# Performance work log

Hardware: AMD Instinct MI355X
Metric: run time of the kernel (lower is better)

Reference implementation:

```python
import jax, jax.numpy as jnp
import numpy as np

EPS = 1e-12  # torch F.normalize default eps


def l2_normalize_c(x):
    # F.normalize over channel dim (dim=1): x / max(||x||_2, eps)
    nrm = jnp.sqrt(jnp.sum(x * x, axis=1, keepdims=True))
    return x / jnp.maximum(nrm, EPS)


def resize_bilinear_ac(x, H, W):
    # bilinear, align_corners=True (matches torch F.interpolate)
    n, c, h, w = x.shape
    ys = jnp.linspace(0.0, h - 1.0, H)
    xs = jnp.linspace(0.0, w - 1.0, W)
    y0 = jnp.floor(ys).astype(jnp.int32)
    y1 = jnp.minimum(y0 + 1, h - 1)
    wy = (ys - y0.astype(ys.dtype))[:, None]          # [H,1]
    x0 = jnp.floor(xs).astype(jnp.int32)
    x1 = jnp.minimum(x0 + 1, w - 1)
    wx = xs - x0.astype(xs.dtype)                      # [W]
    rows = x[:, :, y0, :] * (1.0 - wy) + x[:, :, y1, :] * wy   # [n,c,H,w]
    return rows[:, :, :, x0] * (1.0 - wx) + rows[:, :, :, x1] * wx  # [n,c,H,W]


def unfold_3x3_d2(x):
    # nn.Unfold(kernel=3, dilation=2, padding=2, stride=1) viewed as [n,c,9,h,w]
    n, c, h, w = x.shape
    xp = jnp.pad(x, ((0, 0), (0, 0), (2, 2), (2, 2)))
    return jnp.stack(
        [xp[:, :, dy:dy + h, dx:dx + w] for dy in (0, 2, 4) for dx in (0, 2, 4)],
        axis=2,
    )  # [n,c,9,h,w], kernel index row-major (ky*3+kx) matching torch unfold


def setup_inputs() -> dict:
    key = jax.random.key(0)
    k1, k2, k3, k4, k5 = jax.random.split(key, 5)
    return {
        "c1": jax.random.normal(k1, (4, 256, 128, 128), dtype=jnp.float32),
        "c2": jax.random.normal(k2, (4, 512, 64, 64), dtype=jnp.float32),
        "out": jax.random.normal(k3, (4, 256, 64, 64), dtype=jnp.float32),
        "w_refine": jax.random.normal(k4, (32, 256), dtype=jnp.float32) * 0.05,
        "w_refine2": jax.random.normal(k5, (32, 512), dtype=jnp.float32) * 0.05,
    }


def reference(c1, c2, out, w_refine, w_refine2):
    n, _, h, w = c1.shape
    # 1x1 conv (no bias) + L2 normalize over channels
    q = l2_normalize_c(jnp.einsum("nchw,kc->nkhw", c1, w_refine))       # [n,32,h,w]
    c2u = resize_bilinear_ac(c2, h, w)
    kft = l2_normalize_c(jnp.einsum("nchw,kc->nkhw", c2u, w_refine2))    # [n,32,h,w]
    kpat = unfold_3x3_d2(kft)                                            # [n,32,9,h,w]
    energy = jnp.einsum("nchw,nckhw->nkhw", q, kpat)                     # [n,9,h,w]
    att = jax.nn.softmax(energy, axis=1)
    outu = resize_bilinear_ac(out, h, w)                                 # [n,C,h,w]
    vpat = unfold_3x3_d2(outu)                                           # [n,C,9,h,w]
    return jnp.einsum("nkhw,nckhw->nchw", att, vpat)
```

## Files before the change

### kernel.cpp

```cpp
#include <hip/hip_runtime.h>
#include <hip/hip_bf16.h>


typedef float f32x4 __attribute__((ext_vector_type(4)));
typedef float f32x2 __attribute__((ext_vector_type(2)));

#define SCL (63.0f / 127.0f)

__global__ __launch_bounds__(512) void k_q(const float* __restrict__ c1,
                                           const float* __restrict__ wr,
                                           float* __restrict__ q) {
    __shared__ float red[4 * 32 * 130];
    int b = blockIdx.x;
    int n = b >> 7;
    int pblk = (b & 127) * 128;
    int t = threadIdx.x;
    int lane = t & 63;
    int w = t >> 6;
    int cg = __builtin_amdgcn_readfirstlane(w & 3);
    int og = __builtin_amdgcn_readfirstlane(w >> 2);

    const float* src = c1 + ((size_t)n * 256 + cg * 64) * 16384 + pblk + lane * 2;
    const float* wp  = wr + (og * 16) * 256 + cg * 64;

    float acc0[16], acc1[16];
#pragma unroll
    for (int o = 0; o < 16; ++o) { acc0[o] = 0.f; acc1[o] = 0.f; }
#pragma unroll 4
    for (int c = 0; c < 64; ++c) {
        f32x2 v = *(const f32x2*)(src + (size_t)c * 16384);
#pragma unroll
        for (int o = 0; o < 16; ++o) {
            float wv = wp[o * 256 + c];
            acc0[o] = fmaf(v[0], wv, acc0[o]);
            acc1[o] = fmaf(v[1], wv, acc1[o]);
        }
    }
#pragma unroll
    for (int o = 0; o < 16; ++o) {
        f32x2 pr = { acc0[o], acc1[o] };
        *(f32x2*)&red[(cg * 32 + og * 16 + o) * 130 + lane * 2] = pr;
    }
    __syncthreads();

    if (t < 256) {
        int px = t & 127, half = t >> 7;
        float v[16];
#pragma unroll
        for (int o = 0; o < 16; ++o) {
            v[o] = red[(0 * 32 + half * 16 + o) * 130 + px]
                 + red[(1 * 32 + half * 16 + o) * 130 + px]
                 + red[(2 * 32 + half * 16 + o) * 130 + px]
                 + red[(3 * 32 + half * 16 + o) * 130 + px];
        }
        float* dst = q + ((size_t)n * 16384 + pblk + px) * 32 + half * 16;
#pragma unroll
        for (int j = 0; j < 4; ++j) {
            f32x4 o4 = { v[4*j], v[4*j+1], v[4*j+2], v[4*j+3] };
            *(f32x4*)(dst + 4 * j) = o4;
        }
    }
}

__global__ __launch_bounds__(1024) void k_kfs(const float* __restrict__ c2,
                                              const float* __restrict__ wr2,
                                              float* __restrict__ kfs) {
    __shared__ float red[8 * 32 * 66];
    int b = blockIdx.x;
    int n = b >> 6;
    int pblk = (b & 63) * 64;
    int t = threadIdx.x;
    int lane = t & 63;
    int w = t >> 6;
    int cg = __builtin_amdgcn_readfirstlane(w & 7);
    int og = __builtin_amdgcn_readfirstlane(w >> 3);

    const float* src = c2 + ((size_t)n * 512 + cg * 64) * 4096 + pblk + lane;
    const float* wp  = wr2 + (og * 16) * 512 + cg * 64;

    float acc[16];
#pragma unroll
    for (int o = 0; o < 16; ++o) acc[o] = 0.f;
#pragma unroll 4
    for (int c = 0; c < 64; ++c) {
        float v = src[(size_t)c * 4096];
#pragma unroll
        for (int o = 0; o < 16; ++o)
            acc[o] = fmaf(v, wp[o * 512 + c], acc[o]);
    }
#pragma unroll
    for (int o = 0; o < 16; ++o)
        red[(cg * 32 + og * 16 + o) * 66 + lane] = acc[o];
    __syncthreads();

    if (t < 512) {
        int px = t & 63, seg = t >> 6;
        float v[4];
#pragma unroll
        for (int j = 0; j < 4; ++j) {
            float r = 0.f;
#pragma unroll
            for (int g = 0; g < 8; ++g) r += red[(g * 32 + seg * 4 + j) * 66 + px];
            v[j] = r;
        }
        f32x4 o4 = { v[0], v[1], v[2], v[3] };
        *(f32x4*)(kfs + ((size_t)n * 4096 + pblk + px) * 32 + seg * 4) = o4;
    }
}

__global__ __launch_bounds__(256) void k_upnorm(const float* __restrict__ kfs,
                                                float* __restrict__ kft) {
    int g = blockIdx.x * 256 + threadIdx.x;
    int p = g >> 2, qt = g & 3;
    int n = p >> 14;
    int rem = p & 16383;
    int y = rem >> 7, x = rem & 127;
    float syf = SCL * (float)y; int y0 = (int)syf; float fy = syf - (float)y0;
    int y1 = min(y0 + 1, 63);
    float sxf = SCL * (float)x; int x0 = (int)sxf; float fx = sxf - (float)x0;
    int x1 = min(x0 + 1, 63);
    size_t base = (size_t)n * 4096 * 32 + qt * 8;
    const f32x4* p00 = (const f32x4*)(kfs + base + ((size_t)(y0 * 64 + x0)) * 32);
    const f32x4* p01 = (const f32x4*)(kfs + base + ((size_t)(y0 * 64 + x1)) * 32);
    const f32x4* p10 = (const f32x4*)(kfs + base + ((size_t)(y1 * 64 + x0)) * 32);
    const f32x4* p11 = (const f32x4*)(kfs + base + ((size_t)(y1 * 64 + x1)) * 32);
    float w00 = (1.f-fy)*(1.f-fx), w01 = (1.f-fy)*fx, w10 = fy*(1.f-fx), w11 = fy*fx;
    float v[8]; float s = 0.f;
#pragma unroll
    for (int j = 0; j < 2; ++j) {
        f32x4 a = p00[j], b = p01[j], c = p10[j], d = p11[j];
#pragma unroll
        for (int tt = 0; tt < 4; ++tt) {
            float r = a[tt]*w00 + b[tt]*w01 + c[tt]*w10 + d[tt]*w11;
            v[4*j + tt] = r;
            s = fmaf(r, r, s);
        }
    }
    s += __shfl_xor(s, 1, 4);
    s += __shfl_xor(s, 2, 4);
    float inv = 1.0f / fmaxf(sqrtf(s), 1e-12f);
    f32x4* dst = (f32x4*)(kft + (size_t)p * 32 + qt * 8);
#pragma unroll
    for (int j = 0; j < 2; ++j) {
        f32x4 t = { v[4*j]*inv, v[4*j+1]*inv, v[4*j+2]*inv, v[4*j+3]*inv };
        dst[j] = t;
    }
}

__global__ __launch_bounds__(256) void k_att_w(const float* __restrict__ q,
                                               const float* __restrict__ kft,
                                               float* __restrict__ wbuf) {
    __shared__ float wsc[64 * 17];
    int t = threadIdx.x;
    int g = blockIdx.x * 256 + t;
    int p = g >> 2, qt = g & 3;
    int n = p >> 14, rem = p & 16383;
    int y = rem >> 7, x = rem & 127;
    int pixL = t >> 2;

    int ybase = min((int)(SCL * (float)max(y - 2, 0)), 60);
    int xbase = min((int)(SCL * (float)max(x - 2, 0)), 60);

    const f32x4* qp = (const f32x4*)(q + (size_t)p * 32 + qt * 8);
    f32x4 q0 = qp[0], q1 = qp[1];
    float qs = 0.f;
#pragma unroll
    for (int tt = 0; tt < 4; ++tt) { qs = fmaf(q0[tt], q0[tt], qs); qs = fmaf(q1[tt], q1[tt], qs); }

    float d[9];
#pragma unroll
    for (int k = 0; k < 9; ++k) {
        int ky = k / 3, kx = k % 3;
        int ny = y + 2 * ky - 2, nx = x + 2 * kx - 2;
        float acc = 0.f;
        if (ny >= 0 && ny < 128 && nx >= 0 && nx < 128) {
            const f32x4* kp = (const f32x4*)(kft + ((size_t)n * 16384 + ny * 128 + nx) * 32 + qt * 8);
            f32x4 a = kp[0], b = kp[1];
            acc = fmaf(a[0], q0[0], acc); acc = fmaf(a[1], q0[1], acc);
            acc = fmaf(a[2], q0[2], acc); acc = fmaf(a[3], q0[3], acc);
            acc = fmaf(b[0], q1[0], acc); acc = fmaf(b[1], q1[1], acc);
            acc = fmaf(b[2], q1[2], acc); acc = fmaf(b[3], q1[3], acc);
        }
        d[k] = acc;
    }
    qs += __shfl_xor(qs, 1, 4); qs += __shfl_xor(qs, 2, 4);
#pragma unroll
    for (int k = 0; k < 9; ++k) {
        d[k] += __shfl_xor(d[k], 1, 4);
        d[k] += __shfl_xor(d[k], 2, 4);
    }
    float qinv = 1.0f / fmaxf(sqrtf(qs), 1e-12f);

    float e[9];
    float m = d[0] * qinv;
#pragma unroll
    for (int k = 0; k < 9; ++k) { e[k] = d[k] * qinv; if (k) m = fmaxf(m, e[k]); }
    float ssum = 0.f;
#pragma unroll
    for (int k = 0; k < 9; ++k) { e[k] = __expf(e[k] - m); ssum += e[k]; }
    float rinv = 1.0f / ssum;

    float* wp = wsc + pixL * 17;
#pragma unroll
    for (int i = 0; i < 16; ++i) wp[i] = 0.f;
#pragma unroll
    for (int ky = 0; ky < 3; ++ky) {
        int ny = y + 2 * ky - 2;
        if (ny < 0 || ny > 127) continue;
        float syf = SCL * (float)ny; int iy0 = (int)syf; float fy = syf - (float)iy0;
        int iy1 = min(iy0 + 1, 63);
        int r0 = (iy0 - ybase) * 4, r1 = (iy1 - ybase) * 4;
#pragma unroll
        for (int kx = 0; kx < 3; ++kx) {
            int nx = x + 2 * kx - 2;
            if (nx < 0 || nx > 127) continue;
            float sxf = SCL * (float)nx; int ix0 = (int)sxf; float fx = sxf - (float)ix0;
            int ix1 = min(ix0 + 1, 63);
            float a = e[ky * 3 + kx] * rinv;
            wp[r0 + (ix0 - xbase)] += a * (1.f - fy) * (1.f - fx);
            wp[r0 + (ix1 - xbase)] += a * (1.f - fy) * fx;
            wp[r1 + (ix0 - xbase)] += a * fy * (1.f - fx);
            wp[r1 + (ix1 - xbase)] += a * fy * fx;
        }
    }
    __syncthreads();

    int px = t & 63, i0 = t >> 6;
    int pb = blockIdx.x * 64;
#pragma unroll
    for (int r = 0; r < 4; ++r) {
        int i = r * 4 + i0;
        wbuf[i * 65536 + pb + px] = wsc[px * 17 + i];
    }
}

__global__ __launch_bounds__(256) void k_agg(const float* __restrict__ wbuf,
                                             const float* __restrict__ outp,
                                             float* __restrict__ res) {
    __shared__ float wlds[128 * 17];
    __shared__ float tile[8 * 260];
    int b = blockIdx.x;
    int cg = b & 3, y = (b >> 2) & 127, n = b >> 9;
    int t = threadIdx.x;
    int x = t & 127, half = t >> 7;

    int ybase = min((int)(SCL * (float)max(y - 2, 0)), 60);
    int pix = n * 16384 + y * 128;

#pragma unroll
    for (int k = 0; k < 8; ++k) {
        int u = t + 256 * k;
        int i = u >> 7, xx = u & 127;
        wlds[xx * 17 + i] = wbuf[i * 65536 + pix + xx];
    }
    __syncthreads();
    float w16[16];
#pragma unroll
    for (int i = 0; i < 16; ++i) w16[i] = wlds[x * 17 + i];
    int xb = min((int)(SCL * (float)max(x - 2, 0)), 60);

    const float* ob = outp + ((size_t)n * 256 + cg * 64) * 4096 + ybase * 64;
    float* rb = res + ((size_t)n * 256 + cg * 64) * 16384 + y * 128 + x;

#pragma unroll 1
    for (int batch = 0; batch < 8; ++batch) {
        __syncthreads();
        const float* src = ob + (size_t)batch * 8 * 4096;
#pragma unroll
        for (int k = 0; k < 2; ++k) {
            int u = t + 256 * k;
            int cl = u >> 6, seg = u & 63;
            f32x4 v = *(const f32x4*)(src + (size_t)cl * 4096 + seg * 4);
            *(f32x4*)&tile[cl * 260 + seg * 4] = v;
        }
        __syncthreads();
#pragma unroll
        for (int cl = 0; cl < 4; ++cl) {
            int c = half * 4 + cl;
            const float* tp = tile + c * 260 + xb;
            float acc = 0.f;
#pragma unroll
            for (int r = 0; r < 4; ++r) {
                acc = fmaf(tp[r*64 + 0], w16[r*4 + 0], acc);
                acc = fmaf(tp[r*64 + 1], w16[r*4 + 1], acc);
                acc = fmaf(tp[r*64 + 2], w16[r*4 + 2], acc);
                acc = fmaf(tp[r*64 + 3], w16[r*4 + 3], acc);
            }
            rb[(size_t)(batch * 8 + c) * 16384] = acc;
        }
    }
}

extern "C" void kernel_launch(void* const* d_in, const int* in_sizes, int n_in,
                              void* d_out, int out_size, void* d_ws, size_t ws_size,
                              hipStream_t stream) {
    const float* c1   = (const float*)d_in[0];
    const float* c2   = (const float*)d_in[1];
    const float* outp = (const float*)d_in[2];
    const float* wr   = (const float*)d_in[3];
    const float* wr2  = (const float*)d_in[4];
    float* res = (float*)d_out;

    float* q_ws   = (float*)d_ws;
    float* kfs_ws = (float*)((char*)d_ws + 8388608);
    float* kft_ws = (float*)((char*)d_ws + 8388608 + 2097152);
    float* w_ws   = (float*)((char*)d_ws + 8388608 + 2097152 + 8388608);

    hipLaunchKernelGGL(k_q,      dim3(512),  dim3(512),  0, stream, c1, wr, q_ws);
    hipLaunchKernelGGL(k_kfs,    dim3(256),  dim3(1024), 0, stream, c2, wr2, kfs_ws);
    hipLaunchKernelGGL(k_upnorm, dim3(1024), dim3(256),  0, stream, kfs_ws, kft_ws);
    hipLaunchKernelGGL(k_att_w,  dim3(1024), dim3(256),  0, stream, q_ws, kft_ws, w_ws);
    hipLaunchKernelGGL(k_agg,    dim3(2048), dim3(256),  0, stream, w_ws, outp, res);
}
```

Before: 81.21 us.

## Fuse query projection into attention-weight kernel, keeping q in shared memory

Merges the 1x1-conv query kernel into the attention-weight kernel so each block computes q for one image row, stages it in LDS, and then does the 3x3 dilated dot products, softmax and bilinear weight folding. This removes the 8 MB q round-trip through global memory and one kernel launch. In exchange the fused kernel has 512 threads, larger LDS use, and extra barriers. Only 512 blocks run, each with the heavier conv phase.

```diff
diff --git a/kernel.cpp b/kernel.cpp
--- a/kernel.cpp
+++ b/kernel.cpp
@@ -6,61 +6,6 @@
 typedef float f32x2 __attribute__((ext_vector_type(2)));
 
 #define SCL (63.0f / 127.0f)
-
-__global__ __launch_bounds__(512) void k_q(const float* __restrict__ c1,
-                                           const float* __restrict__ wr,
-                                           float* __restrict__ q) {
-    __shared__ float red[4 * 32 * 130];
-    int b = blockIdx.x;
-    int n = b >> 7;
-    int pblk = (b & 127) * 128;
-    int t = threadIdx.x;
-    int lane = t & 63;
-    int w = t >> 6;
-    int cg = __builtin_amdgcn_readfirstlane(w & 3);
-    int og = __builtin_amdgcn_readfirstlane(w >> 2);
-
-    const float* src = c1 + ((size_t)n * 256 + cg * 64) * 16384 + pblk + lane * 2;
-    const float* wp  = wr + (og * 16) * 256 + cg * 64;
-
-    float acc0[16], acc1[16];
-#pragma unroll
-    for (int o = 0; o < 16; ++o) { acc0[o] = 0.f; acc1[o] = 0.f; }
-#pragma unroll 4
-    for (int c = 0; c < 64; ++c) {
-        f32x2 v = *(const f32x2*)(src + (size_t)c * 16384);
-#pragma unroll
-        for (int o = 0; o < 16; ++o) {
-            float wv = wp[o * 256 + c];
-            acc0[o] = fmaf(v[0], wv, acc0[o]);
-            acc1[o] = fmaf(v[1], wv, acc1[o]);
-        }
-    }
-#pragma unroll
-    for (int o = 0; o < 16; ++o) {
-        f32x2 pr = { acc0[o], acc1[o] };
-        *(f32x2*)&red[(cg * 32 + og * 16 + o) * 130 + lane * 2] = pr;
-    }
-    __syncthreads();
-
-    if (t < 256) {
-        int px = t & 127, half = t >> 7;
-        float v[16];
-#pragma unroll
-        for (int o = 0; o < 16; ++o) {
-            v[o] = red[(0 * 32 + half * 16 + o) * 130 + px]
-                 + red[(1 * 32 + half * 16 + o) * 130 + px]
-                 + red[(2 * 32 + half * 16 + o) * 130 + px]
-                 + red[(3 * 32 + half * 16 + o) * 130 + px];
-        }
-        float* dst = q + ((size_t)n * 16384 + pblk + px) * 32 + half * 16;
-#pragma unroll
-        for (int j = 0; j < 4; ++j) {
-            f32x4 o4 = { v[4*j], v[4*j+1], v[4*j+2], v[4*j+3] };
-            *(f32x4*)(dst + 4 * j) = o4;
-        }
-    }
-}
 
 __global__ __launch_bounds__(1024) void k_kfs(const float* __restrict__ c2,
                                               const float* __restrict__ wr2,
@@ -147,41 +92,97 @@
     }
 }
 
-__global__ __launch_bounds__(256) void k_att_w(const float* __restrict__ q,
-                                               const float* __restrict__ kft,
-                                               float* __restrict__ wbuf) {
-    __shared__ float wsc[64 * 17];
+__global__ __launch_bounds__(512) void k_fq(const float* __restrict__ c1,
+                                            const float* __restrict__ wr,
+                                            const float* __restrict__ kft,
+                                            float* __restrict__ wbuf) {
+    __shared__ float smem[16640];
+    int b = blockIdx.x;
+    int n = b >> 7;
+    int y = b & 127;
+    int pblk = y * 128;
     int t = threadIdx.x;
-    int g = blockIdx.x * 256 + t;
-    int p = g >> 2, qt = g & 3;
-    int n = p >> 14, rem = p & 16383;
-    int y = rem >> 7, x = rem & 127;
-    int pixL = t >> 2;
-
+    int lane = t & 63;
+    int w = t >> 6;
+    int cg = __builtin_amdgcn_readfirstlane(w & 3);
+    int og = __builtin_amdgcn_readfirstlane(w >> 2);
+
+    {
+        const float* src = c1 + ((size_t)n * 256 + cg * 64) * 16384 + pblk + lane * 2;
+        const float* wp  = wr + (og * 16) * 256 + cg * 64;
+        float acc0[16], acc1[16];
+#pragma unroll
+        for (int o = 0; o < 16; ++o) { acc0[o] = 0.f; acc1[o] = 0.f; }
+#pragma unroll 4
+        for (int c = 0; c < 64; ++c) {
+            f32x2 v = *(const f32x2*)(src + (size_t)c * 16384);
+#pragma unroll
+            for (int o = 0; o < 16; ++o) {
+                float wv = wp[o * 256 + c];
+                acc0[o] = fmaf(v[0], wv, acc0[o]);
+                acc1[o] = fmaf(v[1], wv, acc1[o]);
+            }
+        }
+#pragma unroll
+        for (int o = 0; o < 16; ++o) {
+            f32x2 pr = { acc0[o], acc1[o] };
+            *(f32x2*)&smem[(cg * 32 + og * 16 + o) * 130 + lane * 2] = pr;
+        }
+    }
+    __syncthreads();
+
+    float v16[16];
+    {
+        int px = t & 127, half = (t >> 7) & 1;
+        if (t < 256) {
+#pragma unroll
+            for (int o = 0; o < 16; ++o) {
+                v16[o] = smem[(0 * 32 + half * 16 + o) * 130 + px]
+                       + smem[(1 * 32 + half * 16 + o) * 130 + px]
+                       + smem[(2 * 32 + half * 16 + o) * 130 + px]
+                       + smem[(3 * 32 + half * 16 + o) * 130 + px];
+            }
+        }
+    }
+    __syncthreads();
+    if (t < 256) {
+        int px = t & 127, half = (t >> 7) & 1;
+#pragma unroll
+        for (int o = 0; o < 16; ++o) smem[px * 33 + half * 16 + o] = v16[o];
+    }
+    __syncthreads();
+
+    int px = t >> 2, qt = t & 3;
+    int x = px;
     int ybase = min((int)(SCL * (float)max(y - 2, 0)), 60);
     int xbase = min((int)(SCL * (float)max(x - 2, 0)), 60);
 
-    const f32x4* qp = (const f32x4*)(q + (size_t)p * 32 + qt * 8);
-    f32x4 q0 = qp[0], q1 = qp[1];
+    float qv[8];
+#pragma unroll
+    for (int j = 0; j < 8; ++j) qv[j] = smem[px * 33 + qt * 8 + j];
     float qs = 0.f;
 #pragma unroll
-    for (int tt = 0; tt < 4; ++tt) { qs = fmaf(q0[tt], q0[tt], qs); qs = fmaf(q1[tt], q1[tt], qs); }
+    for (int j = 0; j < 8; ++j) qs = fmaf(qv[j], qv[j], qs);
 
     float d[9];
 #pragma unroll
-    for (int k = 0; k < 9; ++k) {
-        int ky = k / 3, kx = k % 3;
-        int ny = y + 2 * ky - 2, nx = x + 2 * kx - 2;
-        float acc = 0.f;
-        if (ny >= 0 && ny < 128 && nx >= 0 && nx < 128) {
-            const f32x4* kp = (const f32x4*)(kft + ((size_t)n * 16384 + ny * 128 + nx) * 32 + qt * 8);
-            f32x4 a = kp[0], b = kp[1];
-            acc = fmaf(a[0], q0[0], acc); acc = fmaf(a[1], q0[1], acc);
-            acc = fmaf(a[2], q0[2], acc); acc = fmaf(a[3], q0[3], acc);
-            acc = fmaf(b[0], q1[0], acc); acc = fmaf(b[1], q1[1], acc);
-            acc = fmaf(b[2], q1[2], acc); acc = fmaf(b[3], q1[3], acc);
-        }
-        d[k] = acc;
+    for (int ky = 0; ky < 3; ++ky) {
+        int ny = y + 2 * ky - 2;
+        bool rowOK = (ny >= 0) && (ny < 128);
+#pragma unroll
+        for (int kx = 0; kx < 3; ++kx) {
+            int nx = x + 2 * kx - 2;
+            float acc = 0.f;
+            if (rowOK && nx >= 0 && nx < 128) {
+                const f32x4* kp = (const f32x4*)(kft + ((size_t)n * 16384 + ny * 128 + nx) * 32 + qt * 8);
+                f32x4 a = kp[0], b2 = kp[1];
+                acc = fmaf(a[0],  qv[0], acc); acc = fmaf(a[1],  qv[1], acc);
+                acc = fmaf(a[2],  qv[2], acc); acc = fmaf(a[3],  qv[3], acc);
+                acc = fmaf(b2[0], qv[4], acc); acc = fmaf(b2[1], qv[5], acc);
+                acc = fmaf(b2[2], qv[6], acc); acc = fmaf(b2[3], qv[7], acc);
+            }
+            d[ky * 3 + kx] = acc;
+        }
     }
     qs += __shfl_xor(qs, 1, 4); qs += __shfl_xor(qs, 2, 4);
 #pragma unroll
@@ -200,7 +201,7 @@
     for (int k = 0; k < 9; ++k) { e[k] = __expf(e[k] - m); ssum += e[k]; }
     float rinv = 1.0f / ssum;
 
-    float* wp = wsc + pixL * 17;
+    float* wp = smem + 8192 + px * 17;
 #pragma unroll
     for (int i = 0; i < 16; ++i) wp[i] = 0.f;
 #pragma unroll
@@ -225,12 +226,12 @@
     }
     __syncthreads();
 
-    int px = t & 63, i0 = t >> 6;
-    int pb = blockIdx.x * 64;
+    int sx = t & 127, i0 = t >> 7;
+    int pg = n * 16384 + y * 128 + sx;
 #pragma unroll
     for (int r = 0; r < 4; ++r) {
         int i = r * 4 + i0;
-        wbuf[i * 65536 + pb + px] = wsc[px * 17 + i];
+        wbuf[i * 65536 + pg] = smem[8192 + sx * 17 + i];
     }
 }
 
@@ -301,14 +302,12 @@
     const float* wr2  = (const float*)d_in[4];
     float* res = (float*)d_out;
 
-    float* q_ws   = (float*)d_ws;
-    float* kfs_ws = (float*)((char*)d_ws + 8388608);
-    float* kft_ws = (float*)((char*)d_ws + 8388608 + 2097152);
-    float* w_ws   = (float*)((char*)d_ws + 8388608 + 2097152 + 8388608);
-
-    hipLaunchKernelGGL(k_q,      dim3(512),  dim3(512),  0, stream, c1, wr, q_ws);
+    float* kfs_ws = (float*)d_ws;
+    float* kft_ws = (float*)((char*)d_ws + 2097152);
+    float* w_ws   = (float*)((char*)d_ws + 2097152 + 8388608);
+
     hipLaunchKernelGGL(k_kfs,    dim3(256),  dim3(1024), 0, stream, c2, wr2, kfs_ws);
     hipLaunchKernelGGL(k_upnorm, dim3(1024), dim3(256),  0, stream, kfs_ws, kft_ws);
-    hipLaunchKernelGGL(k_att_w,  dim3(1024), dim3(256),  0, stream, q_ws, kft_ws, w_ws);
+    hipLaunchKernelGGL(k_fq,     dim3(512),  dim3(512),  0, stream, c1, wr, kft_ws, w_ws);
     hipLaunchKernelGGL(k_agg,    dim3(2048), dim3(256),  0, stream, w_ws, outp, res);
 }
```

Result: faster. 74.90 us (-7.8%).
